# Performance work log

Hardware: AMD Instinct MI355X
Metric: run time of the kernel (lower is better)

Reference implementation:

```python
import jax, jax.numpy as jnp
import numpy as np

N = 100000      # nodes
E = 1600000     # edges
D_IN = 100
D_OUT = 100


def _sage(x, src, dst, W_agg, W_root, b):
    """PyG SAGEConv, aggr='mean', root_weight=True:
    out = mean_{j in N(i)} x_j @ W_agg + x_i @ W_root + b
    Aggregation flows source -> target (dst gathers from src)."""
    num_nodes = x.shape[0]
    deg = jax.ops.segment_sum(jnp.ones((src.shape[0],), x.dtype), dst,
                              num_segments=num_nodes)
    agg = jax.ops.segment_sum(x[src], dst, num_segments=num_nodes)  # [N, D]
    agg = agg / jnp.maximum(deg, 1.0)[:, None]
    return agg @ W_agg + x @ W_root + b


def setup_inputs() -> dict:
    key = jax.random.key(0)
    ks = jax.random.split(key, 12)
    s = 0.05
    return {
        "x": jax.random.normal(ks[0], (N, D_IN), jnp.float32),
        "edge_index": jax.random.randint(ks[1], (2, E), 0, N, jnp.int32),
        "edge_weight": jax.random.uniform(ks[2], (E,), jnp.float32),
        "W_sage_agg": jax.random.normal(ks[3], (D_IN, D_OUT), jnp.float32) * s,
        "W_sage_root": jax.random.normal(ks[4], (D_IN, D_OUT), jnp.float32) * s,
        "b_sage": jnp.zeros((D_OUT,), jnp.float32),
        "W_mu_agg": jax.random.normal(ks[5], (D_OUT, D_OUT), jnp.float32) * s,
        "W_mu_root": jax.random.normal(ks[6], (D_OUT, D_OUT), jnp.float32) * s,
        "b_mu": jnp.zeros((D_OUT,), jnp.float32),
        "W_var_agg": jax.random.normal(ks[7], (D_OUT, D_OUT), jnp.float32) * s,
        "W_var_root": jax.random.normal(ks[8], (D_OUT, D_OUT), jnp.float32) * s,
        "b_var": jnp.zeros((D_OUT,), jnp.float32),
    }


def reference(x, edge_index, edge_weight,
              W_sage_agg, W_sage_root, b_sage,
              W_mu_agg, W_mu_root, b_mu,
              W_var_agg, W_var_root, b_var):
    # edge_weight is accepted but unused, matching the torch module.
    src, dst = edge_index[0], edge_index[1]
    feat = jax.nn.relu(_sage(x, src, dst, W_sage_agg, W_sage_root, b_sage))
    mu = _sage(feat, src, dst, W_mu_agg, W_mu_root, b_mu)
    var = _sage(feat, src, dst, W_var_agg, W_var_root, b_var)
    return (mu, var)
```

## Files before the change

### kernel.cpp

```cpp
#include <hip/hip_runtime.h>
#include <cstdint>
#include <cstddef>

#define N_NODES 100000
#define N_EDGES 1600000
#define DIM 100
#define DPAD 128
#define ROWS_ALLOC 100096

#define RPB 128
#define GEMM_GRID (ROWS_ALLOC / RPB)

#define KBUCK 1000
#define NPB   100
#define BCAP  2048
#define EPB   6400

#define PREP_BUCKET_BLOCKS 250
#define PREP_CONVERT_BLOCKS 6250
#define PREP_BW_BLOCKS 48
#define PREP_BIAS_BLOCKS 2
#define PREP_GRID (PREP_BUCKET_BLOCKS + PREP_CONVERT_BLOCKS + PREP_BW_BLOCKS + PREP_BIAS_BLOCKS)

typedef __attribute__((ext_vector_type(8))) short s16x8;
typedef __attribute__((ext_vector_type(8))) unsigned short us8;
typedef __attribute__((ext_vector_type(4))) unsigned short us4;
typedef __attribute__((ext_vector_type(4))) float f32x4;
typedef __attribute__((ext_vector_type(2))) float f32x2;
typedef __attribute__((ext_vector_type(4))) unsigned int u32x4;

static __device__ __forceinline__ float bf2f(unsigned short h) {
    return __uint_as_float(((unsigned)h) << 16);
}
static __device__ __forceinline__ unsigned short f2bf(float f) {
    unsigned u = __float_as_uint(f);
    return (unsigned short)((u + 0x7FFFu + ((u >> 16) & 1u)) >> 16);
}

__global__ __launch_bounds__(256) void prep_fused(const int* __restrict__ ei,
                                                  unsigned* __restrict__ bucket_cur,
                                                  unsigned* __restrict__ regions,
                                                  const float* __restrict__ X,
                                                  unsigned short* __restrict__ Xp,
                                                  const float* __restrict__ W0, const float* __restrict__ W1,
                                                  const float* __restrict__ W2, const float* __restrict__ W3,
                                                  const float* __restrict__ W4, const float* __restrict__ W5,
                                                  unsigned short* __restrict__ Wt,
                                                  const float* __restrict__ b0, const float* __restrict__ b1,
                                                  const float* __restrict__ b2, float* __restrict__ bp) {
    __shared__ unsigned hist[KBUCK];
    __shared__ unsigned posl[KBUCK];
    int bid = blockIdx.x;
    int tid = threadIdx.x;

    if (bid < PREP_BUCKET_BLOCKS) {
        int e0 = bid * EPB;
        for (int i = tid; i < KBUCK; i += 256) hist[i] = 0;
        __syncthreads();
        for (int i = tid; i < EPB; i += 256) {
            int dst = ei[N_EDGES + e0 + i];
            int b = dst / NPB;
            atomicAdd(&hist[b], 1u);
        }
        __syncthreads();
        for (int i = tid; i < KBUCK; i += 256) {
            unsigned h = hist[i];
            posl[i] = h ? atomicAdd(&bucket_cur[i], h) : 0u;
        }
        __syncthreads();
        for (int i = tid; i < EPB; i += 256) {
            int src = ei[e0 + i];
            int dst = ei[N_EDGES + e0 + i];
            int b = dst / NPB;
            int dl = dst - b * NPB;
            unsigned r = atomicAdd(&posl[b], 1u);
            if (r < BCAP) regions[(size_t)b * BCAP + r] = ((unsigned)src << 8) | (unsigned)dl;
        }
    } else if (bid < PREP_BUCKET_BLOCKS + PREP_CONVERT_BLOCKS) {
        int t = (bid - PREP_BUCKET_BLOCKS) * 256 + tid;
        if (t >= N_NODES * 16) return;
        int node = t >> 4, chunk = t & 15;
        us8 o;
        if (chunk < 12) {
            const float4* p = (const float4*)(X + (size_t)node * DIM + chunk * 8);
            float4 a = p[0], b = p[1];
            o[0] = f2bf(a.x); o[1] = f2bf(a.y); o[2] = f2bf(a.z); o[3] = f2bf(a.w);
            o[4] = f2bf(b.x); o[5] = f2bf(b.y); o[6] = f2bf(b.z); o[7] = f2bf(b.w);
        } else if (chunk == 12) {
            const float4* p = (const float4*)(X + (size_t)node * DIM + 96);
            float4 a = p[0];
            o[0] = f2bf(a.x); o[1] = f2bf(a.y); o[2] = f2bf(a.z); o[3] = f2bf(a.w);
            o[4] = 0; o[5] = 0; o[6] = 0; o[7] = 0;
        } else {
            for (int i = 0; i < 8; ++i) o[i] = 0;
        }
        *(us8*)(Xp + (size_t)node * DPAD + chunk * 8) = o;
    } else if (bid < PREP_BUCKET_BLOCKS + PREP_CONVERT_BLOCKS + PREP_BW_BLOCKS) {
        int t = (bid - PREP_BUCKET_BLOCKS - PREP_CONVERT_BLOCKS) * 256 + tid;
        if (t >= 6 * DPAD * 16) return;
        int mat = t / (DPAD * 16);
        int rem = t % (DPAD * 16);
        int nrow = rem >> 4, chunk = rem & 15;
        const float* W = (mat == 0) ? W0 : (mat == 1) ? W1 : (mat == 2) ? W2
                       : (mat == 3) ? W3 : (mat == 4) ? W4 : W5;
        us8 o;
        #pragma unroll
        for (int j = 0; j < 8; ++j) {
            int k = chunk * 8 + j;
            float v = (k < DIM && nrow < DIM) ? W[(size_t)k * DIM + nrow] : 0.f;
            o[j] = f2bf(v);
        }
        *(us8*)(Wt + (size_t)mat * DPAD * DPAD + (size_t)nrow * DPAD + chunk * 8) = o;
    } else {
        int t = (bid - PREP_BUCKET_BLOCKS - PREP_CONVERT_BLOCKS - PREP_BW_BLOCKS) * 256 + tid;
        if (t >= 3 * DPAD) return;
        int mat = t / DPAD, i = t % DPAD;
        const float* b = (mat == 0) ? b0 : (mat == 1) ? b1 : b2;
        bp[t] = (i < DIM) ? b[i] : 0.f;
    }
}

__global__ __launch_bounds__(256) void csr_kernel(const unsigned* __restrict__ regions,
                                                  const unsigned* __restrict__ bucket_cur,
                                                  unsigned* __restrict__ gbase,
                                                  int* __restrict__ row_off,
                                                  int* __restrict__ cnt,
                                                  int* __restrict__ csr_src) {
    __shared__ unsigned hist[256];
    __shared__ unsigned sa[256], sb[256];
    __shared__ unsigned posl[256];
    __shared__ unsigned sh_gb;
    int tid = threadIdx.x;
    int b = blockIdx.x;
    unsigned total = bucket_cur[b];
    if (total > BCAP) total = BCAP;
    hist[tid] = 0;
    __syncthreads();
    const unsigned* reg = regions + (size_t)b * BCAP;
    for (unsigned e = tid; e < total; e += 256)
        atomicAdd(&hist[reg[e] & 0xFFu], 1u);
    __syncthreads();
    unsigned* cur = sa; unsigned* nxt = sb;
    cur[tid] = hist[tid];
    __syncthreads();
    for (int off = 1; off < 256; off <<= 1) {
        unsigned t = cur[tid];
        if (tid >= off) t += cur[tid - off];
        nxt[tid] = t;
        __syncthreads();
        unsigned* tmp = cur; cur = nxt; nxt = tmp;
    }
    unsigned excl = cur[tid] - hist[tid];
    if (tid == 0) sh_gb = atomicAdd(gbase, total);
    __syncthreads();
    unsigned gb = sh_gb;
    posl[tid] = gb + excl;
    if (tid < NPB) {
        int node = b * NPB + tid;
        cnt[node] = (int)hist[tid];
        row_off[node] = (int)(gb + excl);
    }
    __syncthreads();
    for (unsigned e = tid; e < total; e += 256) {
        unsigned p = reg[e];
        unsigned r = atomicAdd(&posl[p & 0xFFu], 1u);
        csr_src[r] = (int)(p >> 8);
    }
}

__global__ __launch_bounds__(256) void aggregate_pad(const unsigned short* __restrict__ Xh,
                                                     const int* __restrict__ csr_src,
                                                     const int* __restrict__ row_off,
                                                     const int* __restrict__ cnt,
                                                     unsigned short* __restrict__ outh, int n) {
    int node = blockIdx.x * 4 + (threadIdx.x >> 6);
    if (node >= n) return;
    int lane  = threadIdx.x & 63;
    int chunk = lane & 15;
    int slot  = lane >> 4;
    int start = row_off[node];
    int deg   = cnt[node];

    f32x2 acc2[4];
    #pragma unroll
    for (int k = 0; k < 4; ++k) acc2[k] = (f32x2){0.f, 0.f};

    const int coff = chunk * 8;
    int base = 0;
    for (; base + 16 <= deg; base += 16) {
        const int* ep = csr_src + start + base + slot * 4;
        int s0 = ep[0], s1 = ep[1], s2 = ep[2], s3 = ep[3];
        u32x4 w0 = *(const u32x4*)(Xh + (size_t)s0 * DPAD + coff);
        u32x4 w1 = *(const u32x4*)(Xh + (size_t)s1 * DPAD + coff);
        u32x4 w2 = *(const u32x4*)(Xh + (size_t)s2 * DPAD + coff);
        u32x4 w3 = *(const u32x4*)(Xh + (size_t)s3 * DPAD + coff);
        #pragma unroll
        for (int k = 0; k < 4; ++k) {
            acc2[k] += (f32x2){__uint_as_float(w0[k] << 16), __uint_as_float(w0[k] & 0xFFFF0000u)};
            acc2[k] += (f32x2){__uint_as_float(w1[k] << 16), __uint_as_float(w1[k] & 0xFFFF0000u)};
            acc2[k] += (f32x2){__uint_as_float(w2[k] << 16), __uint_as_float(w2[k] & 0xFFFF0000u)};
            acc2[k] += (f32x2){__uint_as_float(w3[k] << 16), __uint_as_float(w3[k] & 0xFFFF0000u)};
        }
    }
    if (base < deg) {
        int e0 = base + slot * 4;
        #pragma unroll
        for (int t = 0; t < 4; ++t) {
            int el = e0 + t;
            bool ok = el < deg;
            int eg = start + (ok ? el : (deg - 1));
            int s  = csr_src[eg];
            u32x4 w = *(const u32x4*)(Xh + (size_t)s * DPAD + coff);
            float mval = ok ? 1.f : 0.f;
            f32x2 mm = (f32x2){mval, mval};
            #pragma unroll
            for (int k = 0; k < 4; ++k) {
                f32x2 v = (f32x2){__uint_as_float(w[k] << 16), __uint_as_float(w[k] & 0xFFFF0000u)};
                acc2[k] += v * mm;
            }
        }
    }
    #pragma unroll
    for (int k = 0; k < 4; ++k) {
        acc2[k].x += __shfl_xor(acc2[k].x, 16, 64);
        acc2[k].y += __shfl_xor(acc2[k].y, 16, 64);
        acc2[k].x += __shfl_xor(acc2[k].x, 32, 64);
        acc2[k].y += __shfl_xor(acc2[k].y, 32, 64);
    }
    if (lane < 16) {
        float inv = 1.0f / (float)(deg > 0 ? deg : 1);
        us8 o;
        #pragma unroll
        for (int k = 0; k < 4; ++k) {
            o[2 * k]     = f2bf(acc2[k].x * inv);
            o[2 * k + 1] = f2bf(acc2[k].y * inv);
        }
        *(us8*)(outh + (size_t)node * DPAD + coff) = o;
    }
}

__global__ __launch_bounds__(256, 2) void gemm_l1_strip(const unsigned short* __restrict__ Aagg,
                                                        const unsigned short* __restrict__ Aroot,
                                                        const unsigned short* __restrict__ WtA,
                                                        const unsigned short* __restrict__ WtR,
                                                        const float* __restrict__ bpad,
                                                        unsigned short* __restrict__ outp) {
    int lane  = threadIdx.x & 63;
    int strip = threadIdx.x >> 6;
    int m16   = lane & 15;
    int quad  = lane >> 4;
    int row0  = blockIdx.x * RPB;

    s16x8 wf[2][2][4];
    const unsigned short* Ws[2] = {WtA, WtR};
    #pragma unroll
    for (int ph = 0; ph < 2; ++ph)
        #pragma unroll
        for (int nt = 0; nt < 2; ++nt)
            #pragma unroll
            for (int ks = 0; ks < 4; ++ks)
                wf[ph][nt][ks] = *(const s16x8*)(Ws[ph] + (size_t)(strip * 32 + nt * 16 + m16) * DPAD + ks * 32 + quad * 8);
    #pragma unroll
    for (int ph = 0; ph < 2; ++ph)
        #pragma unroll
        for (int nt = 0; nt < 2; ++nt)
            #pragma unroll
            for (int ks = 0; ks < 4; ++ks)
                asm volatile("" : "+v"(wf[ph][nt][ks]));

    float4 bias4[2];
    #pragma unroll
    for (int nt = 0; nt < 2; ++nt)
        bias4[nt] = *(const float4*)(bpad + strip * 32 + nt * 16 + quad * 4);

    s16x8 bA[2][4], bR[2][4];
    #pragma unroll
    for (int ks = 0; ks < 4; ++ks) {
        bA[0][ks] = *(const s16x8*)(Aagg  + (size_t)(row0 + m16) * DPAD + ks * 32 + quad * 8);
        bR[0][ks] = *(const s16x8*)(Aroot + (size_t)(row0 + m16) * DPAD + ks * 32 + quad * 8);
    }

    #pragma unroll
    for (int t = 0; t < RPB / 16; ++t) {
        int cur = t & 1;
        if (t < RPB / 16 - 1) {
            int mn = row0 + (t + 1) * 16 + m16;
            #pragma unroll
            for (int ks = 0; ks < 4; ++ks) {
                bA[cur ^ 1][ks] = *(const s16x8*)(Aagg  + (size_t)mn * DPAD + ks * 32 + quad * 8);
                bR[cur ^ 1][ks] = *(const s16x8*)(Aroot + (size_t)mn * DPAD + ks * 32 + quad * 8);
            }
        }
        f32x4 acc[2];
        acc[0] = (f32x4){0.f, 0.f, 0.f, 0.f};
        acc[1] = (f32x4){0.f, 0.f, 0.f, 0.f};
        #pragma unroll
        for (int ks = 0; ks < 4; ++ks) {
            acc[0] = __builtin_amdgcn_mfma_f32_16x16x32_bf16(wf[0][0][ks], bA[cur][ks], acc[0], 0, 0, 0);
            acc[1] = __builtin_amdgcn_mfma_f32_16x16x32_bf16(wf[0][1][ks], bA[cur][ks], acc[1], 0, 0, 0);
            acc[0] = __builtin_amdgcn_mfma_f32_16x16x32_bf16(wf[1][0][ks], bR[cur][ks], acc[0], 0, 0, 0);
            acc[1] = __builtin_amdgcn_mfma_f32_16x16x32_bf16(wf[1][1][ks], bR[cur][ks], acc[1], 0, 0, 0);
        }
        int m = row0 + t * 16 + m16;
        #pragma unroll
        for (int nt = 0; nt < 2; ++nt) {
            int col0 = strip * 32 + nt * 16 + quad * 4;
            us4 o;
            #pragma unroll
            for (int r = 0; r < 4; ++r) {
                float v = acc[nt][r] + ((const float*)&bias4[nt])[r];
                v = v > 0.f ? v : 0.f;
                o[r] = f2bf(v);
            }
            *(us4*)(outp + (size_t)m * DPAD + col0) = o;
        }
    }
}

__global__ __launch_bounds__(256, 2) void gemm_l2_strip(const unsigned short* __restrict__ Aagg,
                                                        const unsigned short* __restrict__ Afeat,
                                                        const unsigned short* __restrict__ WtMA,
                                                        const unsigned short* __restrict__ WtMR,
                                                        const unsigned short* __restrict__ WtVA,
                                                        const unsigned short* __restrict__ WtVR,
                                                        const float* __restrict__ bpm,
                                                        const float* __restrict__ bpv,
                                                        float* __restrict__ outMu,
                                                        float* __restrict__ outVar) {
    int lane  = threadIdx.x & 63;
    int strip = threadIdx.x >> 6;
    int m16   = lane & 15;
    int quad  = lane >> 4;
    int row0  = blockIdx.x * RPB;

    s16x8 wf[2][2][2][4];
    const unsigned short* Ws[2][2] = {{WtMA, WtMR}, {WtVA, WtVR}};
    #pragma unroll
    for (int hd = 0; hd < 2; ++hd)
        #pragma unroll
        for (int ph = 0; ph < 2; ++ph)
            #pragma unroll
            for (int nt = 0; nt < 2; ++nt)
                #pragma unroll
                for (int ks = 0; ks < 4; ++ks)
                    wf[hd][ph][nt][ks] = *(const s16x8*)(Ws[hd][ph] + (size_t)(strip * 32 + nt * 16 + m16) * DPAD + ks * 32 + quad * 8);
    #pragma unroll
    for (int hd = 0; hd < 2; ++hd)
        #pragma unroll
        for (int ph = 0; ph < 2; ++ph)
            #pragma unroll
            for (int nt = 0; nt < 2; ++nt)
                #pragma unroll
                for (int ks = 0; ks < 4; ++ks)
                    asm volatile("" : "+v"(wf[hd][ph][nt][ks]));

    float4 bm4[2], bv4[2];
    #pragma unroll
    for (int nt = 0; nt < 2; ++nt) {
        bm4[nt] = *(const float4*)(bpm + strip * 32 + nt * 16 + quad * 4);
        bv4[nt] = *(const float4*)(bpv + strip * 32 + nt * 16 + quad * 4);
    }

    s16x8 bA[2][4], bF[2][4];
    #pragma unroll
    for (int ks = 0; ks < 4; ++ks) {
        bA[0][ks] = *(const s16x8*)(Aagg  + (size_t)(row0 + m16) * DPAD + ks * 32 + quad * 8);
        bF[0][ks] = *(const s16x8*)(Afeat + (size_t)(row0 + m16) * DPAD + ks * 32 + quad * 8);
    }

    #pragma unroll
    for (int t = 0; t < RPB / 16; ++t) {
        int cur = t & 1;
        if (t < RPB / 16 - 1) {
            int mn = row0 + (t + 1) * 16 + m16;
            #pragma unroll
            for (int ks = 0; ks < 4; ++ks) {
                bA[cur ^ 1][ks] = *(const s16x8*)(Aagg  + (size_t)mn * DPAD + ks * 32 + quad * 8);
                bF[cur ^ 1][ks] = *(const s16x8*)(Afeat + (size_t)mn * DPAD + ks * 32 + quad * 8);
            }
        }
        f32x4 aM[2], aV[2];
        aM[0] = (f32x4){0.f,0.f,0.f,0.f}; aM[1] = (f32x4){0.f,0.f,0.f,0.f};
        aV[0] = (f32x4){0.f,0.f,0.f,0.f}; aV[1] = (f32x4){0.f,0.f,0.f,0.f};
        #pragma unroll
        for (int ks = 0; ks < 4; ++ks) {
            aM[0] = __builtin_amdgcn_mfma_f32_16x16x32_bf16(wf[0][0][0][ks], bA[cur][ks], aM[0], 0, 0, 0);
            aM[1] = __builtin_amdgcn_mfma_f32_16x16x32_bf16(wf[0][0][1][ks], bA[cur][ks], aM[1], 0, 0, 0);
            aV[0] = __builtin_amdgcn_mfma_f32_16x16x32_bf16(wf[1][0][0][ks], bA[cur][ks], aV[0], 0, 0, 0);
            aV[1] = __builtin_amdgcn_mfma_f32_16x16x32_bf16(wf[1][0][1][ks], bA[cur][ks], aV[1], 0, 0, 0);
            aM[0] = __builtin_amdgcn_mfma_f32_16x16x32_bf16(wf[0][1][0][ks], bF[cur][ks], aM[0], 0, 0, 0);
            aM[1] = __builtin_amdgcn_mfma_f32_16x16x32_bf16(wf[0][1][1][ks], bF[cur][ks], aM[1], 0, 0, 0);
            aV[0] = __builtin_amdgcn_mfma_f32_16x16x32_bf16(wf[1][1][0][ks], bF[cur][ks], aV[0], 0, 0, 0);
            aV[1] = __builtin_amdgcn_mfma_f32_16x16x32_bf16(wf[1][1][1][ks], bF[cur][ks], aV[1], 0, 0, 0);
        }
        int m = row0 + t * 16 + m16;
        if (m < N_NODES) {
            #pragma unroll
            for (int nt = 0; nt < 2; ++nt) {
                int col0 = strip * 32 + nt * 16 + quad * 4;
                if (col0 <= DIM - 4) {
                    float4 vm, vv;
                    vm.x = aM[nt][0] + bm4[nt].x; vm.y = aM[nt][1] + bm4[nt].y;
                    vm.z = aM[nt][2] + bm4[nt].z; vm.w = aM[nt][3] + bm4[nt].w;
                    vv.x = aV[nt][0] + bv4[nt].x; vv.y = aV[nt][1] + bv4[nt].y;
                    vv.z = aV[nt][2] + bv4[nt].z; vv.w = aV[nt][3] + bv4[nt].w;
                    *(float4*)(outMu  + (size_t)m * DIM + col0) = vm;
                    *(float4*)(outVar + (size_t)m * DIM + col0) = vv;
                }
            }
        }
    }
}

extern "C" void kernel_launch(void* const* d_in, const int* in_sizes, int n_in,
                              void* d_out, int out_size, void* d_ws, size_t ws_size,
                              hipStream_t stream) {
    const float* x   = (const float*)d_in[0];
    const int*   ei  = (const int*)d_in[1];
    const float* Wsa = (const float*)d_in[3];
    const float* Wsr = (const float*)d_in[4];
    const float* bs  = (const float*)d_in[5];
    const float* Wma = (const float*)d_in[6];
    const float* Wmr = (const float*)d_in[7];
    const float* bm  = (const float*)d_in[8];
    const float* Wva = (const float*)d_in[9];
    const float* Wvr = (const float*)d_in[10];
    const float* bv  = (const float*)d_in[11];

    float* out_mu  = (float*)d_out;
    float* out_var = out_mu + (size_t)N_NODES * DIM;

    char* ws = (char*)d_ws;
    int*      row_off    = (int*)(ws);
    int*      cnt        = (int*)(ws + 400000);
    unsigned* bucket_cur = (unsigned*)(ws + 800000);
    unsigned* gbase      = (unsigned*)(ws + 804096);
    int*      csr_src    = (int*)(ws + 804224);
    unsigned short* Wt   = (unsigned short*)(ws + 7204224);
    float*          bp   = (float*)(ws + 7400832);
    unsigned short* xp   = (unsigned short*)(ws + 7402496);
    unsigned short* aggp = (unsigned short*)(ws + 33027072);
    unsigned short* ftp  = (unsigned short*)(ws + 58651648);
    unsigned* regions    = (unsigned*)(ws + 58651648);

    unsigned short* WtSA = Wt;
    unsigned short* WtSR = Wt + 1 * DPAD * DPAD;
    unsigned short* WtMA = Wt + 2 * DPAD * DPAD;
    unsigned short* WtMR = Wt + 3 * DPAD * DPAD;
    unsigned short* WtVA = Wt + 4 * DPAD * DPAD;
    unsigned short* WtVR = Wt + 5 * DPAD * DPAD;
    float* bps = bp;
    float* bpm = bp + DPAD;
    float* bpv = bp + 2 * DPAD;

    hipMemsetAsync(bucket_cur, 0, 4096, stream);
    hipMemsetAsync(gbase, 0, 128, stream);

    prep_fused<<<PREP_GRID, 256, 0, stream>>>(ei, bucket_cur, regions, x, xp,
                                              Wsa, Wsr, Wma, Wmr, Wva, Wvr, Wt,
                                              bs, bm, bv, bp);
    csr_kernel<<<KBUCK, 256, 0, stream>>>(regions, bucket_cur, gbase, row_off, cnt, csr_src);

    aggregate_pad<<<N_NODES / 4, 256, 0, stream>>>(xp, csr_src, row_off, cnt, aggp, N_NODES);
    gemm_l1_strip<<<GEMM_GRID, 256, 0, stream>>>(aggp, xp, WtSA, WtSR, bps, ftp);

    aggregate_pad<<<N_NODES / 4, 256, 0, stream>>>(ftp, csr_src, row_off, cnt, aggp, N_NODES);
    gemm_l2_strip<<<GEMM_GRID, 256, 0, stream>>>(aggp, ftp, WtMA, WtMR, WtVA, WtVR,
                                                 bpm, bpv, out_mu, out_var);
}
```

Before: 405.6 us.

## Replace bucketed CSR build with global atomic count, three-pass scan and scatter

```diff
diff --git a/kernel.cpp b/kernel.cpp
--- a/kernel.cpp
+++ b/kernel.cpp
@@ -11,16 +11,14 @@
 #define RPB 128
 #define GEMM_GRID (ROWS_ALLOC / RPB)
 
-#define KBUCK 1000
-#define NPB   100
-#define BCAP  2048
-#define EPB   6400
-
-#define PREP_BUCKET_BLOCKS 250
+#define EDGE_BLOCKS 1563
+#define SCAN_BLOCKS 391
+
+#define PREP_COUNT_BLOCKS 1563
 #define PREP_CONVERT_BLOCKS 6250
 #define PREP_BW_BLOCKS 48
 #define PREP_BIAS_BLOCKS 2
-#define PREP_GRID (PREP_BUCKET_BLOCKS + PREP_CONVERT_BLOCKS + PREP_BW_BLOCKS + PREP_BIAS_BLOCKS)
+#define PREP_GRID (PREP_COUNT_BLOCKS + PREP_CONVERT_BLOCKS + PREP_BW_BLOCKS + PREP_BIAS_BLOCKS)
 
 typedef __attribute__((ext_vector_type(8))) short s16x8;
 typedef __attribute__((ext_vector_type(8))) unsigned short us8;
@@ -38,8 +36,7 @@
 }
 
 __global__ __launch_bounds__(256) void prep_fused(const int* __restrict__ ei,
-                                                  unsigned* __restrict__ bucket_cur,
-                                                  unsigned* __restrict__ regions,
+                                                  int* __restrict__ cnt,
                                                   const float* __restrict__ X,
                                                   unsigned short* __restrict__ Xp,
                                                   const float* __restrict__ W0, const float* __restrict__ W1,
@@ -48,36 +45,18 @@
                                                   unsigned short* __restrict__ Wt,
                                                   const float* __restrict__ b0, const float* __restrict__ b1,
                                                   const float* __restrict__ b2, float* __restrict__ bp) {
-    __shared__ unsigned hist[KBUCK];
-    __shared__ unsigned posl[KBUCK];
     int bid = blockIdx.x;
     int tid = threadIdx.x;
 
-    if (bid < PREP_BUCKET_BLOCKS) {
-        int e0 = bid * EPB;
-        for (int i = tid; i < KBUCK; i += 256) hist[i] = 0;
-        __syncthreads();
-        for (int i = tid; i < EPB; i += 256) {
-            int dst = ei[N_EDGES + e0 + i];
-            int b = dst / NPB;
-            atomicAdd(&hist[b], 1u);
-        }
-        __syncthreads();
-        for (int i = tid; i < KBUCK; i += 256) {
-            unsigned h = hist[i];
-            posl[i] = h ? atomicAdd(&bucket_cur[i], h) : 0u;
-        }
-        __syncthreads();
-        for (int i = tid; i < EPB; i += 256) {
-            int src = ei[e0 + i];
-            int dst = ei[N_EDGES + e0 + i];
-            int b = dst / NPB;
-            int dl = dst - b * NPB;
-            unsigned r = atomicAdd(&posl[b], 1u);
-            if (r < BCAP) regions[(size_t)b * BCAP + r] = ((unsigned)src << 8) | (unsigned)dl;
-        }
-    } else if (bid < PREP_BUCKET_BLOCKS + PREP_CONVERT_BLOCKS) {
-        int t = (bid - PREP_BUCKET_BLOCKS) * 256 + tid;
+    if (bid < PREP_COUNT_BLOCKS) {
+        int e0 = bid * 1024;
+        #pragma unroll
+        for (int j = 0; j < 4; ++j) {
+            int e = e0 + j * 256 + tid;
+            if (e < N_EDGES) atomicAdd(&cnt[ei[N_EDGES + e]], 1);
+        }
+    } else if (bid < PREP_COUNT_BLOCKS + PREP_CONVERT_BLOCKS) {
+        int t = (bid - PREP_COUNT_BLOCKS) * 256 + tid;
         if (t >= N_NODES * 16) return;
         int node = t >> 4, chunk = t & 15;
         us8 o;
@@ -95,8 +74,8 @@
             for (int i = 0; i < 8; ++i) o[i] = 0;
         }
         *(us8*)(Xp + (size_t)node * DPAD + chunk * 8) = o;
-    } else if (bid < PREP_BUCKET_BLOCKS + PREP_CONVERT_BLOCKS + PREP_BW_BLOCKS) {
-        int t = (bid - PREP_BUCKET_BLOCKS - PREP_CONVERT_BLOCKS) * 256 + tid;
+    } else if (bid < PREP_COUNT_BLOCKS + PREP_CONVERT_BLOCKS + PREP_BW_BLOCKS) {
+        int t = (bid - PREP_COUNT_BLOCKS - PREP_CONVERT_BLOCKS) * 256 + tid;
         if (t >= 6 * DPAD * 16) return;
         int mat = t / (DPAD * 16);
         int rem = t % (DPAD * 16);
@@ -112,7 +91,7 @@
         }
         *(us8*)(Wt + (size_t)mat * DPAD * DPAD + (size_t)nrow * DPAD + chunk * 8) = o;
     } else {
-        int t = (bid - PREP_BUCKET_BLOCKS - PREP_CONVERT_BLOCKS - PREP_BW_BLOCKS) * 256 + tid;
+        int t = (bid - PREP_COUNT_BLOCKS - PREP_CONVERT_BLOCKS - PREP_BW_BLOCKS) * 256 + tid;
         if (t >= 3 * DPAD) return;
         int mat = t / DPAD, i = t % DPAD;
         const float* b = (mat == 0) ? b0 : (mat == 1) ? b1 : b2;
@@ -120,29 +99,49 @@
     }
 }
 
-__global__ __launch_bounds__(256) void csr_kernel(const unsigned* __restrict__ regions,
-                                                  const unsigned* __restrict__ bucket_cur,
-                                                  unsigned* __restrict__ gbase,
-                                                  int* __restrict__ row_off,
-                                                  int* __restrict__ cnt,
-                                                  int* __restrict__ csr_src) {
-    __shared__ unsigned hist[256];
-    __shared__ unsigned sa[256], sb[256];
-    __shared__ unsigned posl[256];
-    __shared__ unsigned sh_gb;
+__global__ __launch_bounds__(256) void scan_part(const int* __restrict__ cnt,
+                                                 unsigned* __restrict__ bsum) {
+    __shared__ unsigned red[256];
     int tid = threadIdx.x;
-    int b = blockIdx.x;
-    unsigned total = bucket_cur[b];
-    if (total > BCAP) total = BCAP;
-    hist[tid] = 0;
+    int i = blockIdx.x * 256 + tid;
+    unsigned v = (i < N_NODES) ? (unsigned)cnt[i] : 0u;
+    red[tid] = v;
     __syncthreads();
-    const unsigned* reg = regions + (size_t)b * BCAP;
-    for (unsigned e = tid; e < total; e += 256)
-        atomicAdd(&hist[reg[e] & 0xFFu], 1u);
+    for (int off = 128; off > 0; off >>= 1) {
+        if (tid < off) red[tid] += red[tid + off];
+        __syncthreads();
+    }
+    if (tid == 0) bsum[blockIdx.x] = red[0];
+}
+
+__global__ __launch_bounds__(512) void scan_top(const unsigned* __restrict__ bsum,
+                                                unsigned* __restrict__ bpre) {
+    __shared__ unsigned sa[512], sb[512];
+    int tid = threadIdx.x;
+    unsigned v = (tid < SCAN_BLOCKS) ? bsum[tid] : 0u;
+    sa[tid] = v;
     __syncthreads();
     unsigned* cur = sa; unsigned* nxt = sb;
-    cur[tid] = hist[tid];
+    for (int off = 1; off < 512; off <<= 1) {
+        unsigned t = cur[tid];
+        if (tid >= off) t += cur[tid - off];
+        nxt[tid] = t;
+        __syncthreads();
+        unsigned* tmp = cur; cur = nxt; nxt = tmp;
+    }
+    if (tid < SCAN_BLOCKS) bpre[tid] = cur[tid] - v;
+}
+
+__global__ __launch_bounds__(256) void scan_apply(const int* __restrict__ cnt,
+                                                  const unsigned* __restrict__ bpre,
+                                                  int* __restrict__ row_off) {
+    __shared__ unsigned sa[256], sb[256];
+    int tid = threadIdx.x;
+    int i = blockIdx.x * 256 + tid;
+    unsigned v = (i < N_NODES) ? (unsigned)cnt[i] : 0u;
+    sa[tid] = v;
     __syncthreads();
+    unsigned* cur = sa; unsigned* nxt = sb;
     for (int off = 1; off < 256; off <<= 1) {
         unsigned t = cur[tid];
         if (tid >= off) t += cur[tid - off];
@@ -150,21 +149,23 @@
         __syncthreads();
         unsigned* tmp = cur; cur = nxt; nxt = tmp;
     }
-    unsigned excl = cur[tid] - hist[tid];
-    if (tid == 0) sh_gb = atomicAdd(gbase, total);
-    __syncthreads();
-    unsigned gb = sh_gb;
-    posl[tid] = gb + excl;
-    if (tid < NPB) {
-        int node = b * NPB + tid;
-        cnt[node] = (int)hist[tid];
-        row_off[node] = (int)(gb + excl);
-    }
-    __syncthreads();
-    for (unsigned e = tid; e < total; e += 256) {
-        unsigned p = reg[e];
-        unsigned r = atomicAdd(&posl[p & 0xFFu], 1u);
-        csr_src[r] = (int)(p >> 8);
+    if (i < N_NODES) row_off[i] = (int)(bpre[blockIdx.x] + cur[tid] - v);
+}
+
+__global__ __launch_bounds__(256) void scatter_kernel(const int* __restrict__ ei,
+                                                      int* __restrict__ row_off,
+                                                      int* __restrict__ csr_src) {
+    int tid = threadIdx.x;
+    int e0 = blockIdx.x * 1024;
+    #pragma unroll
+    for (int j = 0; j < 4; ++j) {
+        int e = e0 + j * 256 + tid;
+        if (e < N_EDGES) {
+            int s = ei[e];
+            int d = ei[N_EDGES + e];
+            int r = atomicAdd(&row_off[d], 1);
+            csr_src[r] = s;
+        }
     }
 }
 
@@ -178,8 +179,8 @@
     int lane  = threadIdx.x & 63;
     int chunk = lane & 15;
     int slot  = lane >> 4;
-    int start = row_off[node];
     int deg   = cnt[node];
+    int start = row_off[node] - deg;
 
     f32x2 acc2[4];
     #pragma unroll
@@ -433,15 +434,14 @@
     char* ws = (char*)d_ws;
     int*      row_off    = (int*)(ws);
     int*      cnt        = (int*)(ws + 400000);
-    unsigned* bucket_cur = (unsigned*)(ws + 800000);
-    unsigned* gbase      = (unsigned*)(ws + 804096);
+    unsigned* bsum       = (unsigned*)(ws + 800000);
+    unsigned* bpre       = (unsigned*)(ws + 802048);
     int*      csr_src    = (int*)(ws + 804224);
     unsigned short* Wt   = (unsigned short*)(ws + 7204224);
     float*          bp   = (float*)(ws + 7400832);
     unsigned short* xp   = (unsigned short*)(ws + 7402496);
     unsigned short* aggp = (unsigned short*)(ws + 33027072);
     unsigned short* ftp  = (unsigned short*)(ws + 58651648);
-    unsigned* regions    = (unsigned*)(ws + 58651648);
 
     unsigned short* WtSA = Wt;
     unsigned short* WtSR = Wt + 1 * DPAD * DPAD;
@@ -453,13 +453,15 @@
     float* bpm = bp + DPAD;
     float* bpv = bp + 2 * DPAD;
 
-    hipMemsetAsync(bucket_cur, 0, 4096, stream);
-    hipMemsetAsync(gbase, 0, 128, stream);
-
-    prep_fused<<<PREP_GRID, 256, 0, stream>>>(ei, bucket_cur, regions, x, xp,
+    hipMemsetAsync(cnt, 0, 400000, stream);
+
+    prep_fused<<<PREP_GRID, 256, 0, stream>>>(ei, cnt, x, xp,
                                               Wsa, Wsr, Wma, Wmr, Wva, Wvr, Wt,
                                               bs, bm, bv, bp);
-    csr_kernel<<<KBUCK, 256, 0, stream>>>(regions, bucket_cur, gbase, row_off, cnt, csr_src);
+    scan_part<<<SCAN_BLOCKS, 256, 0, stream>>>(cnt, bsum);
+    scan_top<<<1, 512, 0, stream>>>(bsum, bpre);
+    scan_apply<<<SCAN_BLOCKS, 256, 0, stream>>>(cnt, bpre, row_off);
+    scatter_kernel<<<EDGE_BLOCKS, 256, 0, stream>>>(ei, row_off, csr_src);
 
     aggregate_pad<<<N_NODES / 4, 256, 0, stream>>>(xp, csr_src, row_off, cnt, aggp, N_NODES);
     gemm_l1_strip<<<GEMM_GRID, 256, 0, stream>>>(aggp, xp, WtSA, WtSR, bps, ftp);
```

Result: slower. 529.8 us (+30.6%).
